# Optimization experiments

Measured on AMD Instinct MI355X. Metric: run time of the kernel, lower is better.

The kernel has to match this reference:

```python
import jax, jax.numpy as jnp
import numpy as np

B = 64
FEATS = [96, 64, 64, 64]   # per-level input features
NCNT = [1, 8, 64, 512]     # per-level node counts
NODES = 512                # nodes at current depth (tree[-1])
DEG = 8                    # branching degree at this depth
IN_F = 64                  # features[depth]
OUT_F = 64                 # features[depth+1]
SUP = 640                  # in_f * 10 support hidden


def setup_inputs() -> dict:
    key = jax.random.key(0)
    ks = jax.random.split(key, 12)
    inp = {}
    for i in range(4):
        inp[f"x{i}"] = jax.random.normal(ks[i], (B, NCNT[i], FEATS[i]), jnp.float32)
        inp[f"W{i}"] = jax.random.normal(ks[4 + i], (FEATS[i], OUT_F), jnp.float32) / np.sqrt(FEATS[i]).astype(np.float32)
    inp["branch"] = jax.random.normal(ks[8], (NODES, IN_F, IN_F * DEG), jnp.float32) / np.float32(8.0)
    inp["Ws1"] = jax.random.normal(ks[9], (IN_F, SUP), jnp.float32) / np.float32(8.0)
    inp["Ws2"] = jax.random.normal(ks[10], (SUP, OUT_F), jnp.float32) / np.sqrt(SUP).astype(np.float32)
    bound = np.float32(1.0 / np.sqrt(OUT_F))
    inp["bias"] = jax.random.uniform(ks[11], (1, DEG, OUT_F), jnp.float32, -bound, bound)
    return inp


def _lrelu(v):
    return jnp.where(v > 0, v, 0.2 * v)


def reference(x0, x1, x2, x3, W0, W1, W2, W3, branch, Ws1, Ws2, bias):
    xs = [x0, x1, x2, x3]
    Ws = [W0, W1, W2, W3]
    # multi-depth linear sum: project each ancestor level, replicate each
    # node's vector contiguously down to `NODES` rows (torch repeat+view)
    y = jnp.zeros((B, NODES, OUT_F), jnp.float32)
    for x, W in zip(xs, Ws):
        t = x @ W                                   # (B, n_i, OUT_F)
        y = y + jnp.repeat(t, NODES // t.shape[1], axis=1)
    # branching: per-node weight slice (GEMV per node, shared over batch)
    xb = _lrelu(jnp.einsum('bnf,nfg->bng', x3, branch))  # (B, NODES, IN_F*DEG)
    xb = xb.reshape(B, NODES * DEG, IN_F)
    xb = (xb @ Ws1) @ Ws2                           # support MLP -> (B, NODES*DEG, OUT_F)
    y = xb + jnp.repeat(y, DEG, axis=1)             # y repeat(1,1,deg).view
    y = _lrelu(y + jnp.tile(bias, (1, NODES, 1)))   # bias.repeat(1, nodes, 1)
    return y
```

## Files before the change

kernel.cpp:

```cpp
#include <hip/hip_runtime.h>


typedef float f32x4 __attribute__((ext_vector_type(4)));
typedef __bf16 bf16x8 __attribute__((ext_vector_type(8)));

__device__ __forceinline__ unsigned short f2bf(float f) {
    union { float f; unsigned int u; } x; x.f = f;
    unsigned int r = x.u + 0x7FFFu + ((x.u >> 16) & 1u);
    return (unsigned short)(r >> 16);
}

__global__ __launch_bounds__(256) void tree_prep(
    const float* __restrict__ x0, const float* __restrict__ W0,
    const float* __restrict__ x1, const float* __restrict__ W1,
    const float* __restrict__ x2, const float* __restrict__ W2,
    const float* __restrict__ x3, const float* __restrict__ W3,
    const float* __restrict__ Ws1, const float* __restrict__ Ws2,
    float* __restrict__ ylg, unsigned short* __restrict__ xbf,
    unsigned short* __restrict__ wsF, unsigned short* __restrict__ w3f)
{
    const int t = threadIdx.x;
    const int blk = blockIdx.x;
    if (blk < 1024) {
        const int b = blk >> 4;
        const int g = ((blk & 15) << 2) + (t >> 6);
        const int f = t & 63;
        const float* xp = x0 + b * 96;
        float a0 = 0.f, a1 = 0.f;
        #pragma unroll 8
        for (int k = 0; k < 96; k += 2) {
            a0 += xp[k]     * W0[k * 64 + f];
            a1 += xp[k + 1] * W0[(k + 1) * 64 + f];
        }
        const float* x1p = x1 + b * 512 + (g >> 3) * 64;
        #pragma unroll 8
        for (int k = 0; k < 64; k += 2) {
            a0 += x1p[k]     * W1[k * 64 + f];
            a1 += x1p[k + 1] * W1[(k + 1) * 64 + f];
        }
        const float* x2p = x2 + b * 4096 + g * 64;
        #pragma unroll 8
        for (int k = 0; k < 64; k += 2) {
            a0 += x2p[k]     * W2[k * 64 + f];
            a1 += x2p[k + 1] * W2[(k + 1) * 64 + f];
        }
        const int mt = b >> 4, l4 = (b >> 2) & 3, r = b & 3;
        const int ft = f >> 4, l15 = f & 15;
        ylg[(size_t)((g * 4 + mt) * 4 + ft) * 256 + (l4 * 16 + l15) * 4 + r] = a0 + a1;
    } else if (blk < 3072) {
        const int bb = blk - 1024;
        const int b = bb >> 5, ngrp = bb & 31;
        const int n = ngrp * 16 + (t >> 4), k0 = 4 * (t & 15);
        float4 v = *(const float4*)(x3 + (size_t)b * 32768 + (size_t)n * 64 + k0);
        const int mt = b >> 4, l15b = b & 15, ks = k0 >> 5, l4k = (k0 >> 3) & 3, j = k0 & 7;
        union { unsigned short h[4]; uint2 u; } p;
        p.h[0] = f2bf(v.x); p.h[1] = f2bf(v.y); p.h[2] = f2bf(v.z); p.h[3] = f2bf(v.w);
        *(uint2*)&xbf[(size_t)n * 4096 + ((mt * 2 + ks) * 64 + l4k * 16 + l15b) * 8 + j] = p.u;
    } else if (blk < 3136) {
        __shared__ float red[4][64];
        const int c = blk - 3072;
        const int f = t & 63, q = t >> 6;
        const float* w1p = Ws1 + (size_t)c * 640 + q * 160;
        const float* w2p = Ws2 + (size_t)(q * 160) * 64 + f;
        float a0 = 0.f, a1 = 0.f;
        #pragma unroll 8
        for (int s = 0; s < 160; s += 2) {
            a0 += w1p[s]     * w2p[(size_t)s * 64];
            a1 += w1p[s + 1] * w2p[(size_t)(s + 1) * 64];
        }
        red[q][f] = a0 + a1;
        __syncthreads();
        if (q == 0) {
            const float v = red[0][f] + red[1][f] + red[2][f] + red[3][f];
            const int ks = c >> 5, l4c = (c >> 3) & 3, j = c & 7;
            wsF[((f >> 4) * 2 + ks) * 512 + (l4c * 16 + (f & 15)) * 8 + j] = f2bf(v);
        }
    } else {
        const int l = t & 63;
        #pragma unroll
        for (int it = 0; it < 2; ++it) {
            const int fh = it * 4 + (t >> 6);
            const int ft = fh >> 1, ks = fh & 1;
            const int f = ft * 16 + (l & 15);
            const int kb = ks * 32 + (l >> 4) * 8;
            union { unsigned short h[8]; uint4 u; } p;
            #pragma unroll
            for (int j = 0; j < 8; ++j) p.h[j] = f2bf(W3[(kb + j) * 64 + f]);
            *(uint4*)&w3f[((size_t)fh * 64 + l) * 8] = p.u;
        }
    }
}

__global__ __launch_bounds__(64, 2) void tree_main(
    const float* __restrict__ branch, const float* __restrict__ bias,
    const float* __restrict__ ylg, const unsigned short* __restrict__ xbf,
    const unsigned short* __restrict__ wsF, const unsigned short* __restrict__ w3f,
    float* __restrict__ out)
{
    __shared__ unsigned short Ts[64 * 72];
    const int l = threadIdx.x;
    const int l15 = l & 15, l4 = l >> 4;
    const int n = blockIdx.x >> 3, d = blockIdx.x & 7;
    const int g = n >> 3;

    const float* bp = branch + (size_t)n * 32768 + d * 64 + l15;
    float br[4][2][8];
    #pragma unroll
    for (int ct = 0; ct < 4; ++ct)
        #pragma unroll
        for (int ks = 0; ks < 2; ++ks)
            #pragma unroll
            for (int j = 0; j < 8; ++j)
                br[ct][ks][j] = bp[(size_t)(ks * 32 + 8 * l4 + j) * 512 + 16 * ct];

    bf16x8 af[4][2];
    #pragma unroll
    for (int mt = 0; mt < 4; ++mt)
        #pragma unroll
        for (int ks = 0; ks < 2; ++ks)
            af[mt][ks] = *(const bf16x8*)(xbf + (size_t)n * 4096 +
                                          ((mt * 2 + ks) * 64 + l) * 8);

    bf16x8 w3[4][2];
    #pragma unroll
    for (int ft = 0; ft < 4; ++ft)
        #pragma unroll
        for (int ks = 0; ks < 2; ++ks)
            w3[ft][ks] = *(const bf16x8*)(w3f + (size_t)((ft * 2 + ks) * 64 + l) * 8);

    f32x4 y[4][4];
    #pragma unroll
    for (int mt = 0; mt < 4; ++mt)
        #pragma unroll
        for (int ft = 0; ft < 4; ++ft)
            y[mt][ft] = *(const f32x4*)(ylg + (size_t)((g * 4 + mt) * 4 + ft) * 256 + l * 4);
    #pragma unroll
    for (int mt = 0; mt < 4; ++mt)
        #pragma unroll
        for (int ft = 0; ft < 4; ++ft) {
            y[mt][ft] = __builtin_amdgcn_mfma_f32_16x16x32_bf16(af[mt][0], w3[ft][0], y[mt][ft], 0, 0, 0);
            y[mt][ft] = __builtin_amdgcn_mfma_f32_16x16x32_bf16(af[mt][1], w3[ft][1], y[mt][ft], 0, 0, 0);
        }

    #pragma unroll
    for (int ct = 0; ct < 4; ++ct) {
        union { unsigned short h[8]; bf16x8 bv; } p0, p1;
        #pragma unroll
        for (int j = 0; j < 8; ++j) { p0.h[j] = f2bf(br[ct][0][j]); p1.h[j] = f2bf(br[ct][1][j]); }
        #pragma unroll
        for (int mt = 0; mt < 4; ++mt) {
            f32x4 s = {0.f, 0.f, 0.f, 0.f};
            s = __builtin_amdgcn_mfma_f32_16x16x32_bf16(af[mt][0], p0.bv, s, 0, 0, 0);
            s = __builtin_amdgcn_mfma_f32_16x16x32_bf16(af[mt][1], p1.bv, s, 0, 0, 0);
            #pragma unroll
            for (int r = 0; r < 4; ++r) {
                float v = s[r];
                v = fmaxf(v, 0.2f * v);
                Ts[(16 * mt + 4 * l4 + r) * 72 + 16 * ct + l15] = f2bf(v);
            }
        }
    }

    bf16x8 wf[4][2];
    #pragma unroll
    for (int ft = 0; ft < 4; ++ft)
        #pragma unroll
        for (int ks = 0; ks < 2; ++ks)
            wf[ft][ks] = *(const bf16x8*)(wsF + (size_t)((ft * 2 + ks) * 64 + l) * 8);

    float* outp = out + (size_t)blockIdx.x * 64;
    #pragma unroll
    for (int mt = 0; mt < 4; ++mt) {
        bf16x8 at0 = *(const bf16x8*)&Ts[(16 * mt + l15) * 72 + 8 * l4];
        bf16x8 at1 = *(const bf16x8*)&Ts[(16 * mt + l15) * 72 + 32 + 8 * l4];
        #pragma unroll
        for (int ft = 0; ft < 4; ++ft) {
            f32x4 o = {0.f, 0.f, 0.f, 0.f};
            o = __builtin_amdgcn_mfma_f32_16x16x32_bf16(at0, wf[ft][0], o, 0, 0, 0);
            o = __builtin_amdgcn_mfma_f32_16x16x32_bf16(at1, wf[ft][1], o, 0, 0, 0);
            const float bv = bias[d * 64 + 16 * ft + l15];
            #pragma unroll
            for (int r = 0; r < 4; ++r) {
                float val = o[r] + y[mt][ft][r] + bv;
                val = fmaxf(val, 0.2f * val);
                outp[(size_t)(16 * mt + 4 * l4 + r) * 262144 + 16 * ft + l15] = val;
            }
        }
    }
}

extern "C" void kernel_launch(void* const* d_in, const int* in_sizes, int n_in,
                              void* d_out, int out_size, void* d_ws, size_t ws_size,
                              hipStream_t stream) {
    (void)in_sizes; (void)n_in; (void)out_size; (void)ws_size;
    const float* x0     = (const float*)d_in[0];
    const float* W0     = (const float*)d_in[1];
    const float* x1     = (const float*)d_in[2];
    const float* W1     = (const float*)d_in[3];
    const float* x2     = (const float*)d_in[4];
    const float* W2     = (const float*)d_in[5];
    const float* x3     = (const float*)d_in[6];
    const float* W3     = (const float*)d_in[7];
    const float* branch = (const float*)d_in[8];
    const float* Ws1    = (const float*)d_in[9];
    const float* Ws2    = (const float*)d_in[10];
    const float* bias   = (const float*)d_in[11];

    float* ylg          = (float*)d_ws;
    unsigned short* xbf = (unsigned short*)((char*)d_ws + 1048576);
    unsigned short* wsF = (unsigned short*)((char*)d_ws + 5242880);
    unsigned short* w3f = (unsigned short*)((char*)d_ws + 5251072);
    float* out = (float*)d_out;

    tree_prep<<<3137, 256, 0, stream>>>(x0, W0, x1, W1, x2, W2, x3, W3, Ws1, Ws2,
                                        ylg, xbf, wsF, w3f);
    tree_main<<<4096, 64, 0, stream>>>(branch, bias, ylg, xbf, wsF, w3f, out);
}
```

Measured before the change: 54.37 us.

## Stage branch slices through LDS with float4 loads and fold y-MFMA into epilogue

The branch weight slice is now loaded with coalesced float4 reads, converted to bf16 and transposed through a small LDS tile one column group at a time. This replaces the 64 scalar strided loads per lane that were held in registers. The y projection MFMAs and their ylg loads move into the output loop, so they accumulate into the same tile as the support product instead of keeping a full 4x4 accumulator array live. The lower register pressure allows raising the launch bound to three blocks per SIMD, at the cost of extra LDS traffic and more barrier-free LDS reuse within the wave.

```diff
diff --git a/kernel.cpp b/kernel.cpp
--- a/kernel.cpp
+++ b/kernel.cpp
@@ -91,27 +91,26 @@
     }
 }
 
-__global__ __launch_bounds__(64, 2) void tree_main(
+__global__ __launch_bounds__(64, 3) void tree_main(
     const float* __restrict__ branch, const float* __restrict__ bias,
     const float* __restrict__ ylg, const unsigned short* __restrict__ xbf,
     const unsigned short* __restrict__ wsF, const unsigned short* __restrict__ w3f,
     float* __restrict__ out)
 {
+    __shared__ unsigned short Bt[16 * 72];
     __shared__ unsigned short Ts[64 * 72];
     const int l = threadIdx.x;
     const int l15 = l & 15, l4 = l >> 4;
     const int n = blockIdx.x >> 3, d = blockIdx.x & 7;
     const int g = n >> 3;
-
-    const float* bp = branch + (size_t)n * 32768 + d * 64 + l15;
-    float br[4][2][8];
-    #pragma unroll
-    for (int ct = 0; ct < 4; ++ct)
-        #pragma unroll
-        for (int ks = 0; ks < 2; ++ks)
-            #pragma unroll
-            for (int j = 0; j < 8; ++j)
-                br[ct][ks][j] = bp[(size_t)(ks * 32 + 8 * l4 + j) * 512 + 16 * ct];
+    const int rk = l & 15, cq = l >> 4;
+
+    const float* brp = branch + (size_t)n * 32768 + d * 64 + 4 * cq;
+
+    float4 bl[4];
+    #pragma unroll
+    for (int i = 0; i < 4; ++i)
+        bl[i] = *(const float4*)(brp + (size_t)(4 * rk + i) * 512);
 
     bf16x8 af[4][2];
     #pragma unroll
@@ -121,37 +120,27 @@
             af[mt][ks] = *(const bf16x8*)(xbf + (size_t)n * 4096 +
                                           ((mt * 2 + ks) * 64 + l) * 8);
 
-    bf16x8 w3[4][2];
-    #pragma unroll
-    for (int ft = 0; ft < 4; ++ft)
-        #pragma unroll
-        for (int ks = 0; ks < 2; ++ks)
-            w3[ft][ks] = *(const bf16x8*)(w3f + (size_t)((ft * 2 + ks) * 64 + l) * 8);
-
-    f32x4 y[4][4];
-    #pragma unroll
-    for (int mt = 0; mt < 4; ++mt)
-        #pragma unroll
-        for (int ft = 0; ft < 4; ++ft)
-            y[mt][ft] = *(const f32x4*)(ylg + (size_t)((g * 4 + mt) * 4 + ft) * 256 + l * 4);
-    #pragma unroll
-    for (int mt = 0; mt < 4; ++mt)
-        #pragma unroll
-        for (int ft = 0; ft < 4; ++ft) {
-            y[mt][ft] = __builtin_amdgcn_mfma_f32_16x16x32_bf16(af[mt][0], w3[ft][0], y[mt][ft], 0, 0, 0);
-            y[mt][ft] = __builtin_amdgcn_mfma_f32_16x16x32_bf16(af[mt][1], w3[ft][1], y[mt][ft], 0, 0, 0);
-        }
-
     #pragma unroll
     for (int ct = 0; ct < 4; ++ct) {
-        union { unsigned short h[8]; bf16x8 bv; } p0, p1;
-        #pragma unroll
-        for (int j = 0; j < 8; ++j) { p0.h[j] = f2bf(br[ct][0][j]); p1.h[j] = f2bf(br[ct][1][j]); }
+        #pragma unroll
+        for (int ci = 0; ci < 4; ++ci) {
+            union { unsigned short h[4]; uint2 u; } q;
+            #pragma unroll
+            for (int i = 0; i < 4; ++i) q.h[i] = f2bf(((const float*)&bl[i])[ci]);
+            *(uint2*)&Bt[(4 * cq + ci) * 72 + 4 * rk] = q.u;
+        }
+        if (ct < 3) {
+            #pragma unroll
+            for (int i = 0; i < 4; ++i)
+                bl[i] = *(const float4*)(brp + (size_t)(4 * rk + i) * 512 + 16 * (ct + 1));
+        }
+        bf16x8 bt0 = *(const bf16x8*)&Bt[l15 * 72 + 8 * l4];
+        bf16x8 bt1 = *(const bf16x8*)&Bt[l15 * 72 + 32 + 8 * l4];
         #pragma unroll
         for (int mt = 0; mt < 4; ++mt) {
             f32x4 s = {0.f, 0.f, 0.f, 0.f};
-            s = __builtin_amdgcn_mfma_f32_16x16x32_bf16(af[mt][0], p0.bv, s, 0, 0, 0);
-            s = __builtin_amdgcn_mfma_f32_16x16x32_bf16(af[mt][1], p1.bv, s, 0, 0, 0);
+            s = __builtin_amdgcn_mfma_f32_16x16x32_bf16(af[mt][0], bt0, s, 0, 0, 0);
+            s = __builtin_amdgcn_mfma_f32_16x16x32_bf16(af[mt][1], bt1, s, 0, 0, 0);
             #pragma unroll
             for (int r = 0; r < 4; ++r) {
                 float v = s[r];
@@ -161,31 +150,42 @@
         }
     }
 
-    bf16x8 wf[4][2];
+    bf16x8 w3[4][2], wf[4][2];
     #pragma unroll
     for (int ft = 0; ft < 4; ++ft)
         #pragma unroll
-        for (int ks = 0; ks < 2; ++ks)
+        for (int ks = 0; ks < 2; ++ks) {
+            w3[ft][ks] = *(const bf16x8*)(w3f + (size_t)((ft * 2 + ks) * 64 + l) * 8);
             wf[ft][ks] = *(const bf16x8*)(wsF + (size_t)((ft * 2 + ks) * 64 + l) * 8);
+        }
+    float bv[4];
+    #pragma unroll
+    for (int ft = 0; ft < 4; ++ft) bv[ft] = bias[d * 64 + 16 * ft + l15];
 
     float* outp = out + (size_t)blockIdx.x * 64;
     #pragma unroll
     for (int mt = 0; mt < 4; ++mt) {
+        f32x4 y[4];
+        #pragma unroll
+        for (int ft = 0; ft < 4; ++ft)
+            y[ft] = *(const f32x4*)(ylg + (size_t)((g * 4 + mt) * 4 + ft) * 256 + l * 4);
         bf16x8 at0 = *(const bf16x8*)&Ts[(16 * mt + l15) * 72 + 8 * l4];
         bf16x8 at1 = *(const bf16x8*)&Ts[(16 * mt + l15) * 72 + 32 + 8 * l4];
         #pragma unroll
         for (int ft = 0; ft < 4; ++ft) {
-            f32x4 o = {0.f, 0.f, 0.f, 0.f};
-            o = __builtin_amdgcn_mfma_f32_16x16x32_bf16(at0, wf[ft][0], o, 0, 0, 0);
-            o = __builtin_amdgcn_mfma_f32_16x16x32_bf16(at1, wf[ft][1], o, 0, 0, 0);
-            const float bv = bias[d * 64 + 16 * ft + l15];
+            y[ft] = __builtin_amdgcn_mfma_f32_16x16x32_bf16(af[mt][0], w3[ft][0], y[ft], 0, 0, 0);
+            y[ft] = __builtin_amdgcn_mfma_f32_16x16x32_bf16(af[mt][1], w3[ft][1], y[ft], 0, 0, 0);
+            y[ft] = __builtin_amdgcn_mfma_f32_16x16x32_bf16(at0, wf[ft][0], y[ft], 0, 0, 0);
+            y[ft] = __builtin_amdgcn_mfma_f32_16x16x32_bf16(at1, wf[ft][1], y[ft], 0, 0, 0);
+        }
+        #pragma unroll
+        for (int ft = 0; ft < 4; ++ft)
             #pragma unroll
             for (int r = 0; r < 4; ++r) {
-                float val = o[r] + y[mt][ft][r] + bv;
+                float val = y[ft][r] + bv[ft];
                 val = fmaxf(val, 0.2f * val);
                 outp[(size_t)(16 * mt + 4 * l4 + r) * 262144 + 16 * ft + l15] = val;
             }
-        }
     }
 }
 
```

Result: no change. 54.04 us (-0.6%).
